# Performance work log

Hardware: AMD Instinct MI355X
Metric: run time of the kernel (lower is better)

The kernel has to match this reference:

```python
import jax, jax.numpy as jnp
import numpy as np

B, T, N, H = 256, 128, 512, 128  # batch, timesteps, input_size (driving series), hidden


def setup_inputs() -> dict:
    key = jax.random.key(0)
    ks = jax.random.split(key, 7)
    p = lambda k, shape: (jax.random.normal(k, shape, dtype=jnp.float32) * 0.05)
    return {
        "X": jax.random.normal(ks[0], (B, T, N), dtype=jnp.float32),
        # attention linear: in_features = 2H + T, out_features = 1 (stored as a vector + scalar bias)
        "attn_w": p(ks[1], (2 * H + T,)),
        "attn_b": p(ks[2], ()),
        # LSTM cell params, PyTorch layout/gate order (i, f, g, o)
        "w_ih": p(ks[3], (4 * H, N)),
        "w_hh": p(ks[4], (4 * H, H)),
        "b_ih": p(ks[5], (4 * H,)),
        "b_hh": p(ks[6], (4 * H,)),
    }


def reference(X, attn_w, attn_b, w_ih, w_hh, b_ih, b_hh):
    Bn, Tn, Nn = X.shape
    Hh = w_hh.shape[1]
    # split the single attention weight row into the h / s / X-row pieces of the concat
    w_h, w_s, w_x = attn_w[:Hh], attn_w[Hh:2 * Hh], attn_w[2 * Hh:]
    Xp = jnp.swapaxes(X, 1, 2)            # [B, N, T]  (X.permute(0,2,1))
    x_score = Xp @ w_x                    # [B, N], time-invariant part of attention logits

    def step(carry, x_t):                 # x_t: [B, N] = X[:, t, :]
        h, c = carry
        # logits[b,i] = w_h.h[b] + w_s.c[b] + w_x.Xp[b,i] + b  (== Linear on the concat)
        score = x_score + (h @ w_h + c @ w_s + attn_b)[:, None]   # [B, N]
        alpha = jax.nn.softmax(score, axis=1)
        x_tilde = alpha * x_t                                      # [B, N]
        gates = x_tilde @ w_ih.T + h @ w_hh.T + b_ih + b_hh        # [B, 4H]
        i, f, g, o = jnp.split(gates, 4, axis=1)
        c_new = jax.nn.sigmoid(f) * c + jax.nn.sigmoid(i) * jnp.tanh(g)
        h_new = jax.nn.sigmoid(o) * jnp.tanh(c_new)
        return (h_new, c_new), (x_tilde, h_new)

    h0 = jnp.zeros((Bn, Hh), X.dtype)
    (_, _), (Xt, Xe) = jax.lax.scan(step, (h0, h0), jnp.swapaxes(X, 0, 1))
    # scan stacks along time -> [T, B, .]; return [B, T, .]
    return jnp.swapaxes(Xt, 0, 1), jnp.swapaxes(Xe, 0, 1)
```

## Files before the change

kernel.cpp:

```cpp
#include <hip/hip_runtime.h>
#include <hip/hip_bf16.h>

#define Bb 256
#define Tt 128
#define Nn 512
#define Hh 128

typedef __attribute__((ext_vector_type(4))) float floatx4;
typedef __attribute__((ext_vector_type(8))) short short8;
typedef _Float16 h2v_t __attribute__((ext_vector_type(2)));

__device__ __forceinline__ unsigned short f2bf(float f) {
  unsigned u = __float_as_uint(f);
  u += 0x7fffu + ((u >> 16) & 1u);
  return (unsigned short)(u >> 16);
}

__device__ __forceinline__ float sigmoid_fast(float x) {
  return __builtin_amdgcn_rcpf(1.f + __expf(-x));
}
__device__ __forceinline__ float tanh_fast(float x) {
  float e = __expf(2.f * x);
  return 1.f - 2.f * __builtin_amdgcn_rcpf(e + 1.f);
}

__device__ __forceinline__ void lds_barrier() {
  asm volatile("s_waitcnt lgkmcnt(0)" ::: "memory");
  __builtin_amdgcn_s_barrier();
  asm volatile("" ::: "memory");
}

__device__ __forceinline__ void async_load16(const void* g, void* lds) {
  __builtin_amdgcn_global_load_lds(
      (const __attribute__((address_space(1))) unsigned int*)g,
      (__attribute__((address_space(3))) unsigned int*)lds, 16, 0, 0);
}

#if __has_builtin(__builtin_amdgcn_fdot2)
#define FDOT2(a, b, c) __builtin_amdgcn_fdot2((a), (b), (c), false)
#else
__device__ __forceinline__ float fdot2_sw(h2v_t a, h2v_t b, float c) {
  return fmaf((float)a.x, (float)b.x, fmaf((float)a.y, (float)b.y, (c)));
}
#define FDOT2(a, b, c) fdot2_sw((a), (b), (c))
#endif

template <int CTRL>
__device__ __forceinline__ float qperm(float x) {
#if __has_builtin(__builtin_amdgcn_update_dpp)
  return __uint_as_float((unsigned)__builtin_amdgcn_update_dpp(
      0, (int)__float_as_uint(x), CTRL, 0xf, 0xf, true));
#else
  return __shfl_xor(x, CTRL == 0xB1 ? 1 : 2, 64);
#endif
}

__global__ void prep_kernel(const float* __restrict__ w_ih,
                            const float* __restrict__ b_ih,
                            const float* __restrict__ b_hh,
                            unsigned short* __restrict__ wb,
                            float* __restrict__ bias) {
  int i = blockIdx.x * 256 + threadIdx.x;
  if (i < 4 * Hh * Nn) wb[i] = f2bf(w_ih[i]);
  if (i < 4 * Hh) bias[i] = b_ih[i] + b_hh[i];
}

__global__ __launch_bounds__(512) void alpha_kernel(const float* __restrict__ X,
                                                    const float* __restrict__ attn_w,
                                                    float* __restrict__ alpha) {
  int b = blockIdx.x;
  int n = threadIdx.x;
  const float* Xb = X + (size_t)b * Tt * Nn + n;
  float acc = 0.f;
#pragma unroll 8
  for (int t = 0; t < Tt; ++t)
    acc = fmaf(Xb[(size_t)t * Nn], attn_w[2 * Hh + t], acc);

  __shared__ float red[512];
  red[n] = acc;
  __syncthreads();
  for (int s = 256; s > 0; s >>= 1) {
    if (n < s) red[n] = fmaxf(red[n], red[n + s]);
    __syncthreads();
  }
  float m = red[0];
  __syncthreads();
  float e = __expf(acc - m);
  red[n] = e;
  __syncthreads();
  for (int s = 256; s > 0; s >>= 1) {
    if (n < s) red[n] += red[n + s];
    __syncthreads();
  }
  alpha[(size_t)b * Nn + n] = e / red[0];
}

__global__ __launch_bounds__(256) void scale_kernel(const float* __restrict__ X,
                                                    const float* __restrict__ alpha,
                                                    float* __restrict__ Xt,
                                                    unsigned short* __restrict__ xtb) {
  size_t i = (size_t)blockIdx.x * 256 + threadIdx.x;
  size_t e = i * 4;
  int n = (int)(e & (Nn - 1));
  int brow = (int)(e >> 9);
  int b = brow >> 7;
  float4 x = ((const float4*)X)[i];
  float4 a = *(const float4*)(alpha + (size_t)b * Nn + n);
  float4 y;
  y.x = x.x * a.x; y.y = x.y * a.y; y.z = x.z * a.z; y.w = x.w * a.w;
  ((float4*)Xt)[i] = y;
  ushort4 u;
  u.x = f2bf(y.x); u.y = f2bf(y.y); u.z = f2bf(y.z); u.w = f2bf(y.w);
  ((ushort4*)xtb)[i] = u;
}

#define GBK 64

__global__ __launch_bounds__(256) void gemm_bt(const unsigned short* __restrict__ A,
                                               const unsigned short* __restrict__ Bw,
                                               const float* __restrict__ bias,
                                               float* __restrict__ C) {
  __shared__ __align__(16) unsigned short As[128 * 64];
  __shared__ __align__(16) unsigned short Bs[128 * 64];
  const int K = 512, NO = 512;
  int tid = threadIdx.x;
  int lane = tid & 63;
  int wave = tid >> 6;
  int wm = wave & 1, wn = wave >> 1;
  int l15 = lane & 15;
  int quad = lane >> 4;
  int mtile = blockIdx.x, ntile = blockIdx.y;

  floatx4 acc[4][4];
#pragma unroll
  for (int i = 0; i < 4; ++i)
#pragma unroll
    for (int j = 0; j < 4; ++j) acc[i][j] = (floatx4){0.f, 0.f, 0.f, 0.f};

  int lr = lane >> 3;
  int lc = (lane & 7) ^ lr;
  const size_t lane_goff = (size_t)lr * K + lc * 8;
  const size_t abase = (size_t)mtile * 128 * K + lane_goff;
  const size_t bbase = (size_t)ntile * 128 * K + lane_goff;
  int sw = (quad ^ (l15 & 7)) * 8;

  for (int kb = 0; kb < K; kb += GBK) {
#pragma unroll
    for (int slot = 0; slot < 4; ++slot) {
      int r0 = slot * 32 + wave * 8;
      async_load16(A + abase + (size_t)r0 * K + kb, &As[r0 * 64]);
      async_load16(Bw + bbase + (size_t)r0 * K + kb, &Bs[r0 * 64]);
    }
    __syncthreads();
#pragma unroll
    for (int kh = 0; kh < 2; ++kh) {
      int sc = sw ^ (kh * 32);
      short8 af[4], bf[4];
#pragma unroll
      for (int i = 0; i < 4; ++i)
        af[i] = *(const short8*)(&As[(wm * 64 + i * 16 + l15) * 64 + sc]);
#pragma unroll
      for (int j = 0; j < 4; ++j)
        bf[j] = *(const short8*)(&Bs[(wn * 64 + j * 16 + l15) * 64 + sc]);
#pragma unroll
      for (int i = 0; i < 4; ++i)
#pragma unroll
        for (int j = 0; j < 4; ++j)
          acc[i][j] = __builtin_amdgcn_mfma_f32_16x16x32_bf16(af[i], bf[j], acc[i][j], 0, 0, 0);
    }
    __syncthreads();
  }

  int m0 = mtile * 128 + wm * 64;
  int n0 = ntile * 128 + wn * 64;
#pragma unroll
  for (int j = 0; j < 4; ++j) {
    int col = n0 + j * 16 + l15;
    float bsum = bias[col];
#pragma unroll
    for (int i = 0; i < 4; ++i) {
      int row = m0 + i * 16 + quad * 4;
#pragma unroll
      for (int r = 0; r < 4; ++r)
        C[(size_t)(row + r) * NO + col] = acc[i][j][r] + bsum;
    }
  }
}

__global__ __launch_bounds__(512, 1) void lstm_kernel(const float* __restrict__ G,
                                                      const float* __restrict__ w_hh,
                                                      float* __restrict__ Xe) {
  int b = blockIdx.x;
  int tid = threadIdx.x;
  int u = tid >> 2;
  int q = tid & 3;

  h2v_t wreg[4][16];
#pragma unroll
  for (int f = 0; f < 4; ++f) {
    const float4* wr = (const float4*)(w_hh + ((size_t)(f * 128 + u) * 128 + q * 32));
#pragma unroll
    for (int i = 0; i < 8; ++i) {
      float4 v = wr[i];
      wreg[f][2 * i]     = (h2v_t){(_Float16)v.x, (_Float16)v.y};
      wreg[f][2 * i + 1] = (h2v_t){(_Float16)v.z, (_Float16)v.w};
    }
  }

  __shared__ __align__(16) unsigned short h2[2][128];
  if (tid < 128) h2[0][tid] = 0;
  __syncthreads();

  const float* Gb = G + (size_t)b * Tt * 512 + q * 128 + u;
  float* Xeb = Xe + (size_t)b * Tt * Hh;

  float gcur = Gb[0];
  float gnext = Gb[512];
  float c0 = 0.f;

  for (int t = 0; t < Tt; ++t) {
    int cur = t & 1;
    const uint4* hp = (const uint4*)(&h2[cur][0]) + q * 4;
    uint4 ha = hp[0], hb = hp[1], hc = hp[2], hd = hp[3];

    float g_this = gcur;
    gcur = gnext;
    if (t + 2 < Tt) gnext = Gb[(size_t)(t + 2) * 512];

    float pg0 = (q == 0) ? g_this : 0.f;
    float pg1 = (q == 1) ? g_this : 0.f;
    float pg2 = (q == 2) ? g_this : 0.f;
    float pg3 = (q == 3) ? g_this : 0.f;

#define DOTK(HB, K2)                                                \
  {                                                                 \
    h2v_t hh = __builtin_bit_cast(h2v_t, (HB));                     \
    pg0 = FDOT2(hh, wreg[0][K2], pg0);                              \
    pg1 = FDOT2(hh, wreg[1][K2], pg1);                              \
    pg2 = FDOT2(hh, wreg[2][K2], pg2);                              \
    pg3 = FDOT2(hh, wreg[3][K2], pg3);                              \
  }
    DOTK(ha.x, 0)  DOTK(ha.y, 1)  DOTK(ha.z, 2)  DOTK(ha.w, 3)
    DOTK(hb.x, 4)  DOTK(hb.y, 5)  DOTK(hb.z, 6)  DOTK(hb.w, 7)
    DOTK(hc.x, 8)  DOTK(hc.y, 9)  DOTK(hc.z, 10) DOTK(hc.w, 11)
    DOTK(hd.x, 12) DOTK(hd.y, 13) DOTK(hd.z, 14) DOTK(hd.w, 15)
#undef DOTK

    pg0 += qperm<0xB1>(pg0); pg1 += qperm<0xB1>(pg1);
    pg2 += qperm<0xB1>(pg2); pg3 += qperm<0xB1>(pg3);
    pg0 += qperm<0x4E>(pg0); pg1 += qperm<0x4E>(pg1);
    pg2 += qperm<0x4E>(pg2); pg3 += qperm<0x4E>(pg3);

    float si = sigmoid_fast(pg0);
    float sf = sigmoid_fast(pg1);
    float tg = tanh_fast(pg2);
    float so = sigmoid_fast(pg3);
    c0 = sf * c0 + si * tg;
    float hv = so * tanh_fast(c0);

    if (q == 0) {
      Xeb[(size_t)t * Hh + u] = hv;
      h2[cur ^ 1][u] = __builtin_bit_cast(unsigned short, (_Float16)hv);
    }
    lds_barrier();
  }
}

extern "C" void kernel_launch(void* const* d_in, const int* in_sizes, int n_in,
                              void* d_out, int out_size, void* d_ws, size_t ws_size,
                              hipStream_t stream) {
  const float* X      = (const float*)d_in[0];
  const float* attn_w = (const float*)d_in[1];
  const float* w_ih   = (const float*)d_in[3];
  const float* w_hh   = (const float*)d_in[4];
  const float* b_ih   = (const float*)d_in[5];
  const float* b_hh   = (const float*)d_in[6];

  float* Xt = (float*)d_out;
  float* Xe = (float*)d_out + (size_t)Bb * Tt * Nn;

  char* ws = (char*)d_ws;
  float*          alpha = (float*)(ws);
  float*          bias  = (float*)(ws + 524288);
  unsigned short* wb    = (unsigned short*)(ws + 526336);
  unsigned short* xtb   = (unsigned short*)(ws + 1050624);
  float*          G     = (float*)(ws + 34605056);

  prep_kernel<<<dim3(1024), dim3(256), 0, stream>>>(w_ih, b_ih, b_hh, wb, bias);
  alpha_kernel<<<dim3(Bb), dim3(512), 0, stream>>>(X, attn_w, alpha);
  scale_kernel<<<dim3(16384), dim3(256), 0, stream>>>(X, alpha, Xt, xtb);
  gemm_bt<<<dim3(256, 4), dim3(256), 0, stream>>>(xtb, wb, bias, G);
  lstm_kernel<<<dim3(Bb), dim3(512), 0, stream>>>(G, w_hh, Xe);
}
```

Before: 274.0 us.

## Split LSTM gates across quad lanes and vectorize attention softmax kernel

```diff
diff --git a/kernel.cpp b/kernel.cpp
--- a/kernel.cpp
+++ b/kernel.cpp
@@ -46,12 +46,12 @@
 #endif
 
 template <int CTRL>
-__device__ __forceinline__ float qperm(float x) {
+__device__ __forceinline__ float qbcast(float x) {
 #if __has_builtin(__builtin_amdgcn_update_dpp)
   return __uint_as_float((unsigned)__builtin_amdgcn_update_dpp(
       0, (int)__float_as_uint(x), CTRL, 0xf, 0xf, true));
 #else
-  return __shfl_xor(x, CTRL == 0xB1 ? 1 : 2, 64);
+  return __shfl(x, (threadIdx.x & ~3) + (CTRL & 3), 64);
 #endif
 }
 
@@ -69,30 +69,65 @@
                                                     const float* __restrict__ attn_w,
                                                     float* __restrict__ alpha) {
   int b = blockIdx.x;
-  int n = threadIdx.x;
-  const float* Xb = X + (size_t)b * Tt * Nn + n;
-  float acc = 0.f;
+  int tid = threadIdx.x;
+  int c = tid & 127;
+  int tp = tid >> 7;
+  const float4* Xb = (const float4*)(X + (size_t)b * Tt * Nn) + c;
+  const float* wx = attn_w + 2 * Hh;
+
+  float4 acc = {0.f, 0.f, 0.f, 0.f};
 #pragma unroll 8
-  for (int t = 0; t < Tt; ++t)
-    acc = fmaf(Xb[(size_t)t * Nn], attn_w[2 * Hh + t], acc);
-
-  __shared__ float red[512];
-  red[n] = acc;
-  __syncthreads();
-  for (int s = 256; s > 0; s >>= 1) {
-    if (n < s) red[n] = fmaxf(red[n], red[n + s]);
+  for (int tt = 0; tt < 32; ++tt) {
+    int t = tp * 32 + tt;
+    float4 x = Xb[(size_t)t * 128];
+    float w = wx[t];
+    acc.x = fmaf(x.x, w, acc.x);
+    acc.y = fmaf(x.y, w, acc.y);
+    acc.z = fmaf(x.z, w, acc.z);
+    acc.w = fmaf(x.w, w, acc.w);
+  }
+
+  __shared__ float4 s4[512];
+  __shared__ float sred[128];
+  s4[tid] = acc;
+  __syncthreads();
+
+  float4 sc = {0.f, 0.f, 0.f, 0.f};
+  if (tid < 128) {
+    float4 a = s4[tid], b2 = s4[tid + 128], c2 = s4[tid + 256], d = s4[tid + 384];
+    sc.x = a.x + b2.x + c2.x + d.x;
+    sc.y = a.y + b2.y + c2.y + d.y;
+    sc.z = a.z + b2.z + c2.z + d.z;
+    sc.w = a.w + b2.w + c2.w + d.w;
+    sred[tid] = fmaxf(fmaxf(sc.x, sc.y), fmaxf(sc.z, sc.w));
+  }
+  __syncthreads();
+  for (int s = 64; s > 0; s >>= 1) {
+    if (tid < s) sred[tid] = fmaxf(sred[tid], sred[tid + s]);
     __syncthreads();
   }
-  float m = red[0];
-  __syncthreads();
-  float e = __expf(acc - m);
-  red[n] = e;
-  __syncthreads();
-  for (int s = 256; s > 0; s >>= 1) {
-    if (n < s) red[n] += red[n + s];
+  float m = sred[0];
+  __syncthreads();
+
+  float4 e4 = {0.f, 0.f, 0.f, 0.f};
+  if (tid < 128) {
+    e4.x = __expf(sc.x - m);
+    e4.y = __expf(sc.y - m);
+    e4.z = __expf(sc.z - m);
+    e4.w = __expf(sc.w - m);
+    sred[tid] = e4.x + e4.y + e4.z + e4.w;
+  }
+  __syncthreads();
+  for (int s = 64; s > 0; s >>= 1) {
+    if (tid < s) sred[tid] += sred[tid + s];
     __syncthreads();
   }
-  alpha[(size_t)b * Nn + n] = e / red[0];
+  float inv = 1.f / sred[0];
+  if (tid < 128) {
+    float4 out;
+    out.x = e4.x * inv; out.y = e4.y * inv; out.z = e4.z * inv; out.w = e4.w * inv;
+    ((float4*)(alpha + (size_t)b * Nn))[tid] = out;
+  }
 }
 
 __global__ __launch_bounds__(256) void scale_kernel(const float* __restrict__ X,
@@ -193,17 +228,16 @@
   int b = blockIdx.x;
   int tid = threadIdx.x;
   int u = tid >> 2;
-  int q = tid & 3;
-
-  h2v_t wreg[4][16];
-#pragma unroll
-  for (int f = 0; f < 4; ++f) {
-    const float4* wr = (const float4*)(w_hh + ((size_t)(f * 128 + u) * 128 + q * 32));
-#pragma unroll
-    for (int i = 0; i < 8; ++i) {
+  int f = tid & 3;
+
+  h2v_t wreg[64];
+  {
+    const float4* wr = (const float4*)(w_hh + (size_t)(f * 128 + u) * 128);
+#pragma unroll
+    for (int i = 0; i < 32; ++i) {
       float4 v = wr[i];
-      wreg[f][2 * i]     = (h2v_t){(_Float16)v.x, (_Float16)v.y};
-      wreg[f][2 * i + 1] = (h2v_t){(_Float16)v.z, (_Float16)v.w};
+      wreg[2 * i]     = (h2v_t){(_Float16)v.x, (_Float16)v.y};
+      wreg[2 * i + 1] = (h2v_t){(_Float16)v.z, (_Float16)v.w};
     }
   }
 
@@ -211,59 +245,61 @@
   if (tid < 128) h2[0][tid] = 0;
   __syncthreads();
 
-  const float* Gb = G + (size_t)b * Tt * 512 + q * 128 + u;
+  const float* Gb = G + (size_t)b * Tt * 512 + f * 128 + u;
   float* Xeb = Xe + (size_t)b * Tt * Hh;
 
   float gcur = Gb[0];
   float gnext = Gb[512];
   float c0 = 0.f;
 
+  const float actm = (f == 2) ? 2.f : -1.f;
+  const float fA   = (f == 2) ? -2.f : 1.f;
+  const float fB   = (f == 2) ? 1.f : 0.f;
+
+#define H2F(W) __builtin_bit_cast(h2v_t, (W))
+
   for (int t = 0; t < Tt; ++t) {
     int cur = t & 1;
-    const uint4* hp = (const uint4*)(&h2[cur][0]) + q * 4;
-    uint4 ha = hp[0], hb = hp[1], hc = hp[2], hd = hp[3];
+    const uint4* hp = (const uint4*)(&h2[cur][0]);
 
     float g_this = gcur;
     gcur = gnext;
     if (t + 2 < Tt) gnext = Gb[(size_t)(t + 2) * 512];
 
-    float pg0 = (q == 0) ? g_this : 0.f;
-    float pg1 = (q == 1) ? g_this : 0.f;
-    float pg2 = (q == 2) ? g_this : 0.f;
-    float pg3 = (q == 3) ? g_this : 0.f;
-
-#define DOTK(HB, K2)                                                \
-  {                                                                 \
-    h2v_t hh = __builtin_bit_cast(h2v_t, (HB));                     \
-    pg0 = FDOT2(hh, wreg[0][K2], pg0);                              \
-    pg1 = FDOT2(hh, wreg[1][K2], pg1);                              \
-    pg2 = FDOT2(hh, wreg[2][K2], pg2);                              \
-    pg3 = FDOT2(hh, wreg[3][K2], pg3);                              \
-  }
-    DOTK(ha.x, 0)  DOTK(ha.y, 1)  DOTK(ha.z, 2)  DOTK(ha.w, 3)
-    DOTK(hb.x, 4)  DOTK(hb.y, 5)  DOTK(hb.z, 6)  DOTK(hb.w, 7)
-    DOTK(hc.x, 8)  DOTK(hc.y, 9)  DOTK(hc.z, 10) DOTK(hc.w, 11)
-    DOTK(hd.x, 12) DOTK(hd.y, 13) DOTK(hd.z, 14) DOTK(hd.w, 15)
-#undef DOTK
-
-    pg0 += qperm<0xB1>(pg0); pg1 += qperm<0xB1>(pg1);
-    pg2 += qperm<0xB1>(pg2); pg3 += qperm<0xB1>(pg3);
-    pg0 += qperm<0x4E>(pg0); pg1 += qperm<0x4E>(pg1);
-    pg2 += qperm<0x4E>(pg2); pg3 += qperm<0x4E>(pg3);
-
-    float si = sigmoid_fast(pg0);
-    float sf = sigmoid_fast(pg1);
-    float tg = tanh_fast(pg2);
-    float so = sigmoid_fast(pg3);
-    c0 = sf * c0 + si * tg;
-    float hv = so * tanh_fast(c0);
-
-    if (q == 0) {
-      Xeb[(size_t)t * Hh + u] = hv;
-      h2[cur ^ 1][u] = __builtin_bit_cast(unsigned short, (_Float16)hv);
-    }
+    float a0 = g_this, a1 = 0.f;
+#pragma unroll
+    for (int ch = 0; ch < 4; ++ch) {
+      uint4 r0 = hp[ch * 4 + 0], r1 = hp[ch * 4 + 1];
+      uint4 r2 = hp[ch * 4 + 2], r3 = hp[ch * 4 + 3];
+      const h2v_t* wk = &wreg[ch * 16];
+      a0 = FDOT2(H2F(r0.x), wk[0],  a0);  a1 = FDOT2(H2F(r0.y), wk[1],  a1);
+      a0 = FDOT2(H2F(r0.z), wk[2],  a0);  a1 = FDOT2(H2F(r0.w), wk[3],  a1);
+      a0 = FDOT2(H2F(r1.x), wk[4],  a0);  a1 = FDOT2(H2F(r1.y), wk[5],  a1);
+      a0 = FDOT2(H2F(r1.z), wk[6],  a0);  a1 = FDOT2(H2F(r1.w), wk[7],  a1);
+      a0 = FDOT2(H2F(r2.x), wk[8],  a0);  a1 = FDOT2(H2F(r2.y), wk[9],  a1);
+      a0 = FDOT2(H2F(r2.z), wk[10], a0);  a1 = FDOT2(H2F(r2.w), wk[11], a1);
+      a0 = FDOT2(H2F(r3.x), wk[12], a0);  a1 = FDOT2(H2F(r3.y), wk[13], a1);
+      a0 = FDOT2(H2F(r3.z), wk[14], a0);  a1 = FDOT2(H2F(r3.w), wk[15], a1);
+    }
+    float x = a0 + a1;
+
+    float e = __expf(x * actm);
+    float r = __builtin_amdgcn_rcpf(1.f + e);
+    float val = fmaf(r, fA, fB);
+
+    float gi = qbcast<0x00>(val);
+    float gf = qbcast<0x55>(val);
+    float gg = qbcast<0xAA>(val);
+    float go = qbcast<0xFF>(val);
+
+    c0 = fmaf(gf, c0, gi * gg);
+    float hv = go * tanh_fast(c0);
+
+    if (f == 0) h2[cur ^ 1][u] = __builtin_bit_cast(unsigned short, (_Float16)hv);
+    if (f == 1) Xeb[(size_t)t * Hh + u] = hv;
     lds_barrier();
   }
+#undef H2F
 }
 
 extern "C" void kernel_launch(void* const* d_in, const int* in_sizes, int n_in,
```

Result: no change. 276.6 us (+1.0%).
